# Kernel optimization log

Hardware: AMD Instinct MI355X
Metric: run time of the kernel (lower is better)

## Reference

```python
import jax, jax.numpy as jnp
import numpy as np

WEIGHT0 = 1.0
WEIGHT1 = 2.0
N = 33554432

def setup_inputs() -> dict:
    key = jax.random.key(0)
    k1, k2 = jax.random.split(key)
    # probabilities in (0,1); nudge away from exact 0/1 to keep logs finite
    p = jax.random.uniform(k1, (N,), dtype=jnp.float32, minval=1e-6, maxval=1.0 - 1e-6)
    t = jax.random.randint(k2, (N,), 0, 2, dtype=jnp.int32)
    return {"input": p, "target": t}

def reference(input, target):
    # per-element: target==1 -> w1*log(p), else -> w0*log(1-p); loss = -mean
    per_el = jnp.where(target == 1,
                       WEIGHT1 * jnp.log(input),
                       WEIGHT0 * jnp.log1p(-input))
    return -jnp.mean(per_el)
```

## Files before the change

### kernel.cpp

```cpp
#include <hip/hip_runtime.h>


#define W0 1.0f
#define W1 2.0f

#define GRID  2048
#define BLOCK 256

__global__ __launch_bounds__(BLOCK) void bce_reduce_kernel(
    const float* __restrict__ p, const int* __restrict__ t,
    float* __restrict__ partial, int n4) {
  const float4* p4 = (const float4*)p;
  const int4*   t4 = (const int4*)t;

  const int idx    = blockIdx.x * BLOCK + threadIdx.x;
  const int stride = GRID * BLOCK;

  float acc = 0.f;

  int i = idx;
  for (; i + 3 * stride < n4; i += 4 * stride) {
    float4 pv0 = p4[i + 0 * stride];
    float4 pv1 = p4[i + 1 * stride];
    float4 pv2 = p4[i + 2 * stride];
    float4 pv3 = p4[i + 3 * stride];
    int4   tv0 = t4[i + 0 * stride];
    int4   tv1 = t4[i + 1 * stride];
    int4   tv2 = t4[i + 2 * stride];
    int4   tv3 = t4[i + 3 * stride];

    float a0 = 0.f, a1 = 0.f, a2 = 0.f, a3 = 0.f;
    a0 += (tv0.x ? W1 : W0) * __logf(tv0.x ? pv0.x : 1.0f - pv0.x);
    a0 += (tv0.y ? W1 : W0) * __logf(tv0.y ? pv0.y : 1.0f - pv0.y);
    a0 += (tv0.z ? W1 : W0) * __logf(tv0.z ? pv0.z : 1.0f - pv0.z);
    a0 += (tv0.w ? W1 : W0) * __logf(tv0.w ? pv0.w : 1.0f - pv0.w);
    a1 += (tv1.x ? W1 : W0) * __logf(tv1.x ? pv1.x : 1.0f - pv1.x);
    a1 += (tv1.y ? W1 : W0) * __logf(tv1.y ? pv1.y : 1.0f - pv1.y);
    a1 += (tv1.z ? W1 : W0) * __logf(tv1.z ? pv1.z : 1.0f - pv1.z);
    a1 += (tv1.w ? W1 : W0) * __logf(tv1.w ? pv1.w : 1.0f - pv1.w);
    a2 += (tv2.x ? W1 : W0) * __logf(tv2.x ? pv2.x : 1.0f - pv2.x);
    a2 += (tv2.y ? W1 : W0) * __logf(tv2.y ? pv2.y : 1.0f - pv2.y);
    a2 += (tv2.z ? W1 : W0) * __logf(tv2.z ? pv2.z : 1.0f - pv2.z);
    a2 += (tv2.w ? W1 : W0) * __logf(tv2.w ? pv2.w : 1.0f - pv2.w);
    a3 += (tv3.x ? W1 : W0) * __logf(tv3.x ? pv3.x : 1.0f - pv3.x);
    a3 += (tv3.y ? W1 : W0) * __logf(tv3.y ? pv3.y : 1.0f - pv3.y);
    a3 += (tv3.z ? W1 : W0) * __logf(tv3.z ? pv3.z : 1.0f - pv3.z);
    a3 += (tv3.w ? W1 : W0) * __logf(tv3.w ? pv3.w : 1.0f - pv3.w);
    acc += (a0 + a1) + (a2 + a3);
  }
  for (; i < n4; i += stride) {
    float4 pv = p4[i];
    int4   tv = t4[i];
    acc += (tv.x ? W1 : W0) * __logf(tv.x ? pv.x : 1.0f - pv.x);
    acc += (tv.y ? W1 : W0) * __logf(tv.y ? pv.y : 1.0f - pv.y);
    acc += (tv.z ? W1 : W0) * __logf(tv.z ? pv.z : 1.0f - pv.z);
    acc += (tv.w ? W1 : W0) * __logf(tv.w ? pv.w : 1.0f - pv.w);
  }

  #pragma unroll
  for (int off = 32; off > 0; off >>= 1)
    acc += __shfl_down(acc, off, 64);

  __shared__ float s[BLOCK / 64];
  const int wave = threadIdx.x >> 6;
  if ((threadIdx.x & 63) == 0) s[wave] = acc;
  __syncthreads();

  if (threadIdx.x == 0) {
    partial[blockIdx.x] = (s[0] + s[1]) + (s[2] + s[3]);
  }
}

__global__ __launch_bounds__(256) void bce_finalize_kernel(
    const float* __restrict__ partial, float* __restrict__ out, float inv_n) {
  float acc = 0.f;
  for (int i = threadIdx.x; i < GRID; i += 256)
    acc += partial[i];
  #pragma unroll
  for (int off = 32; off > 0; off >>= 1)
    acc += __shfl_down(acc, off, 64);
  __shared__ float s[4];
  const int wave = threadIdx.x >> 6;
  if ((threadIdx.x & 63) == 0) s[wave] = acc;
  __syncthreads();
  if (threadIdx.x == 0)
    out[0] = -((s[0] + s[1]) + (s[2] + s[3])) * inv_n;
}

extern "C" void kernel_launch(void* const* d_in, const int* in_sizes, int n_in,
                              void* d_out, int out_size, void* d_ws, size_t ws_size,
                              hipStream_t stream) {
  const float* p = (const float*)d_in[0];
  const int*   t = (const int*)d_in[1];
  float* out = (float*)d_out;
  float* ws  = (float*)d_ws;

  const int n  = in_sizes[0];
  const int n4 = n / 4;

  bce_reduce_kernel<<<GRID, BLOCK, 0, stream>>>(p, t, ws, n4);
  bce_finalize_kernel<<<1, 256, 0, stream>>>(ws, out, 1.0f / (float)n);
}
```

Before: 278.2 us.

## Fully unroll reduction for exact size with staged prefetch and branchless log2 math

Adds a specialized path for n4 == 16*grid*block in which each thread issues all of its loads in four staged groups, with sched_barriers placed so that later loads overlap compute on earlier ones. The per-element select is replaced by branchless FMA arithmetic that builds p or 1-p from the target value and applies the weight (1+t) through an FMA. The log is computed as log2 and the ln2 factor and negation are folded into the finalize scale, which removes a per-element multiply. Risks are higher register pressure from holding 32 vector loads in flight, and the fast path only fires for one exact input size.

```diff
diff --git a/kernel.cpp b/kernel.cpp
--- a/kernel.cpp
+++ b/kernel.cpp
@@ -1,60 +1,58 @@
 #include <hip/hip_runtime.h>
 
 
-#define W0 1.0f
-#define W1 2.0f
-
 #define GRID  2048
 #define BLOCK 256
+#define LN2F  0.69314718055994531f
 
-__global__ __launch_bounds__(BLOCK) void bce_reduce_kernel(
+__device__ __forceinline__ void acc4(const float4 pv, const int4 tv, float& acc) {
+  float tf0 = (float)tv.x, tf1 = (float)tv.y, tf2 = (float)tv.z, tf3 = (float)tv.w;
+  float x0 = __builtin_fmaf(tf0, __builtin_fmaf(2.f, pv.x, -1.f), 1.f - pv.x);
+  float x1 = __builtin_fmaf(tf1, __builtin_fmaf(2.f, pv.y, -1.f), 1.f - pv.y);
+  float x2 = __builtin_fmaf(tf2, __builtin_fmaf(2.f, pv.z, -1.f), 1.f - pv.z);
+  float x3 = __builtin_fmaf(tf3, __builtin_fmaf(2.f, pv.w, -1.f), 1.f - pv.w);
+  float l0 = __log2f(x0), l1 = __log2f(x1), l2 = __log2f(x2), l3 = __log2f(x3);
+  acc += l0; acc = __builtin_fmaf(tf0, l0, acc);
+  acc += l1; acc = __builtin_fmaf(tf1, l1, acc);
+  acc += l2; acc = __builtin_fmaf(tf2, l2, acc);
+  acc += l3; acc = __builtin_fmaf(tf3, l3, acc);
+}
+
+__global__ __launch_bounds__(BLOCK, 4) void bce_reduce_kernel(
     const float* __restrict__ p, const int* __restrict__ t,
     float* __restrict__ partial, int n4) {
   const float4* p4 = (const float4*)p;
   const int4*   t4 = (const int4*)t;
-
-  const int idx    = blockIdx.x * BLOCK + threadIdx.x;
-  const int stride = GRID * BLOCK;
+  const int idx = blockIdx.x * BLOCK + threadIdx.x;
+  const int S   = GRID * BLOCK;
 
   float acc = 0.f;
 
-  int i = idx;
-  for (; i + 3 * stride < n4; i += 4 * stride) {
-    float4 pv0 = p4[i + 0 * stride];
-    float4 pv1 = p4[i + 1 * stride];
-    float4 pv2 = p4[i + 2 * stride];
-    float4 pv3 = p4[i + 3 * stride];
-    int4   tv0 = t4[i + 0 * stride];
-    int4   tv1 = t4[i + 1 * stride];
-    int4   tv2 = t4[i + 2 * stride];
-    int4   tv3 = t4[i + 3 * stride];
+  if (n4 == 16 * S) {
+    float4 a0 = p4[idx + 0*S], a1 = p4[idx + 1*S], a2 = p4[idx + 2*S], a3 = p4[idx + 3*S];
+    int4   u0 = t4[idx + 0*S], u1 = t4[idx + 1*S], u2 = t4[idx + 2*S], u3 = t4[idx + 3*S];
+    float4 b0 = p4[idx + 4*S], b1 = p4[idx + 5*S], b2 = p4[idx + 6*S], b3 = p4[idx + 7*S];
+    int4   v0 = t4[idx + 4*S], v1 = t4[idx + 5*S], v2 = t4[idx + 6*S], v3 = t4[idx + 7*S];
+    __builtin_amdgcn_sched_barrier(0);
 
-    float a0 = 0.f, a1 = 0.f, a2 = 0.f, a3 = 0.f;
-    a0 += (tv0.x ? W1 : W0) * __logf(tv0.x ? pv0.x : 1.0f - pv0.x);
-    a0 += (tv0.y ? W1 : W0) * __logf(tv0.y ? pv0.y : 1.0f - pv0.y);
-    a0 += (tv0.z ? W1 : W0) * __logf(tv0.z ? pv0.z : 1.0f - pv0.z);
-    a0 += (tv0.w ? W1 : W0) * __logf(tv0.w ? pv0.w : 1.0f - pv0.w);
-    a1 += (tv1.x ? W1 : W0) * __logf(tv1.x ? pv1.x : 1.0f - pv1.x);
-    a1 += (tv1.y ? W1 : W0) * __logf(tv1.y ? pv1.y : 1.0f - pv1.y);
-    a1 += (tv1.z ? W1 : W0) * __logf(tv1.z ? pv1.z : 1.0f - pv1.z);
-    a1 += (tv1.w ? W1 : W0) * __logf(tv1.w ? pv1.w : 1.0f - pv1.w);
-    a2 += (tv2.x ? W1 : W0) * __logf(tv2.x ? pv2.x : 1.0f - pv2.x);
-    a2 += (tv2.y ? W1 : W0) * __logf(tv2.y ? pv2.y : 1.0f - pv2.y);
-    a2 += (tv2.z ? W1 : W0) * __logf(tv2.z ? pv2.z : 1.0f - pv2.z);
-    a2 += (tv2.w ? W1 : W0) * __logf(tv2.w ? pv2.w : 1.0f - pv2.w);
-    a3 += (tv3.x ? W1 : W0) * __logf(tv3.x ? pv3.x : 1.0f - pv3.x);
-    a3 += (tv3.y ? W1 : W0) * __logf(tv3.y ? pv3.y : 1.0f - pv3.y);
-    a3 += (tv3.z ? W1 : W0) * __logf(tv3.z ? pv3.z : 1.0f - pv3.z);
-    a3 += (tv3.w ? W1 : W0) * __logf(tv3.w ? pv3.w : 1.0f - pv3.w);
-    acc += (a0 + a1) + (a2 + a3);
-  }
-  for (; i < n4; i += stride) {
-    float4 pv = p4[i];
-    int4   tv = t4[i];
-    acc += (tv.x ? W1 : W0) * __logf(tv.x ? pv.x : 1.0f - pv.x);
-    acc += (tv.y ? W1 : W0) * __logf(tv.y ? pv.y : 1.0f - pv.y);
-    acc += (tv.z ? W1 : W0) * __logf(tv.z ? pv.z : 1.0f - pv.z);
-    acc += (tv.w ? W1 : W0) * __logf(tv.w ? pv.w : 1.0f - pv.w);
+    acc4(a0, u0, acc); acc4(a1, u1, acc); acc4(a2, u2, acc); acc4(a3, u3, acc);
+    float4 c0 = p4[idx + 8*S], c1 = p4[idx + 9*S], c2 = p4[idx + 10*S], c3 = p4[idx + 11*S];
+    int4   w0 = t4[idx + 8*S], w1 = t4[idx + 9*S], w2 = t4[idx + 10*S], w3 = t4[idx + 11*S];
+    __builtin_amdgcn_sched_barrier(0);
+
+    acc4(b0, v0, acc); acc4(b1, v1, acc); acc4(b2, v2, acc); acc4(b3, v3, acc);
+    float4 d0 = p4[idx + 12*S], d1 = p4[idx + 13*S], d2 = p4[idx + 14*S], d3 = p4[idx + 15*S];
+    int4   z0 = t4[idx + 12*S], z1 = t4[idx + 13*S], z2 = t4[idx + 14*S], z3 = t4[idx + 15*S];
+    __builtin_amdgcn_sched_barrier(0);
+
+    acc4(c0, w0, acc); acc4(c1, w1, acc); acc4(c2, w2, acc); acc4(c3, w3, acc);
+    acc4(d0, z0, acc); acc4(d1, z1, acc); acc4(d2, z2, acc); acc4(d3, z3, acc);
+  } else {
+    for (int i = idx; i < n4; i += S) {
+      float4 pv = p4[i];
+      int4   tv = t4[i];
+      acc4(pv, tv, acc);
+    }
   }
 
   #pragma unroll
@@ -66,13 +64,12 @@
   if ((threadIdx.x & 63) == 0) s[wave] = acc;
   __syncthreads();
 
-  if (threadIdx.x == 0) {
+  if (threadIdx.x == 0)
     partial[blockIdx.x] = (s[0] + s[1]) + (s[2] + s[3]);
-  }
 }
 
 __global__ __launch_bounds__(256) void bce_finalize_kernel(
-    const float* __restrict__ partial, float* __restrict__ out, float inv_n) {
+    const float* __restrict__ partial, float* __restrict__ out, float scale) {
   float acc = 0.f;
   for (int i = threadIdx.x; i < GRID; i += 256)
     acc += partial[i];
@@ -84,7 +81,7 @@
   if ((threadIdx.x & 63) == 0) s[wave] = acc;
   __syncthreads();
   if (threadIdx.x == 0)
-    out[0] = -((s[0] + s[1]) + (s[2] + s[3])) * inv_n;
+    out[0] = ((s[0] + s[1]) + (s[2] + s[3])) * scale;
 }
 
 extern "C" void kernel_launch(void* const* d_in, const int* in_sizes, int n_in,
@@ -99,5 +96,5 @@
   const int n4 = n / 4;
 
   bce_reduce_kernel<<<GRID, BLOCK, 0, stream>>>(p, t, ws, n4);
-  bce_finalize_kernel<<<1, 256, 0, stream>>>(ws, out, 1.0f / (float)n);
+  bce_finalize_kernel<<<1, 256, 0, stream>>>(ws, out, -LN2F / (float)n);
 }
```

Result: no change. 281.8 us (+1.3%).
